# Performance work log

Measured on AMD Instinct MI355X. Metric: run time of the kernel, lower is better.

Reference implementation:

```python
import math
import jax, jax.numpy as jnp
import numpy as np

B, S, H, N = 2, 2048, 2048, 16
HN = H // N
ALPHA = 32.0
MASK_VALUE = 10000.0


def setup_inputs() -> dict:
    key = jax.random.key(0)
    k1, k2, k3, k4, k5 = jax.random.split(key, 5)
    hidden_states = jax.random.normal(k1, (B, S, H), dtype=jnp.float32)
    # causal (left-to-right) multiplicative mask, broadcastable to [b, n, s, s]
    ltor_mask = jnp.tril(jnp.ones((S, S), dtype=jnp.float32))[None, None, :, :]
    # torch Linear params: y = x @ W.T + b
    w_qkv = jax.random.normal(k2, (3 * H, H), dtype=jnp.float32) * (1.0 / math.sqrt(H))
    b_qkv = jnp.zeros((3 * H,), dtype=jnp.float32)
    w_dense = jax.random.normal(k3, (H, H), dtype=jnp.float32) * (1.0 / math.sqrt(H))
    b_dense = jnp.zeros((H,), dtype=jnp.float32)
    return {"hidden_states": hidden_states, "ltor_mask": ltor_mask,
            "w_qkv": w_qkv, "b_qkv": b_qkv, "w_dense": w_dense, "b_dense": b_dense}


def reference(hidden_states, ltor_mask, w_qkv, b_qkv, w_dense, b_dense):
    b, s, h = hidden_states.shape
    # fused qkv projection
    qkv = hidden_states @ w_qkv.T + b_qkv                       # [b, s, 3h]
    q, k, v = jnp.split(qkv, 3, axis=-1)

    def heads(t):  # [b, s, h] -> [b, n, s, hn]
        return t.reshape(b, s, N, HN).transpose(0, 2, 1, 3)

    q, k, v = heads(q), heads(k), heads(v)
    # cogview pb_relax: scale query before matmul
    scores = jnp.einsum('bnsd,bntd->bnst', q / math.sqrt(HN), k)  # [b, n, s, s]
    m = ltor_mask[:, :, -s:]
    scores = scores * m - MASK_VALUE * (1.0 - m)
    # pb_relax max stabilization: per (batch, head) global max of scores/alpha
    scaled = scores / ALPHA
    maxes = jax.lax.stop_gradient(jnp.max(scaled, axis=(-2, -1), keepdims=True))
    scores = (scaled - maxes) * ALPHA
    probs = jax.nn.softmax(scores, axis=-1)
    ctx = jnp.einsum('bnst,bntd->bnsd', probs, v)                # [b, n, s, hn]
    ctx = ctx.transpose(0, 2, 1, 3).reshape(b, s, h)
    out = ctx @ w_dense.T + b_dense
    return out
```

## Files before the change

### kernel.cpp

```cpp
#include <hip/hip_runtime.h>

typedef __bf16 bf16_t;
typedef __bf16 bf16x8 __attribute__((ext_vector_type(8)));
typedef __bf16 bf16x4 __attribute__((ext_vector_type(4)));
typedef float f32x4 __attribute__((ext_vector_type(4)));

#define MFMA16(a, b, c) __builtin_amdgcn_mfma_f32_16x16x32_bf16((a), (b), (c), 0, 0, 0)

__device__ __forceinline__ void gload_lds16(const void* g, void* l) {
  __builtin_amdgcn_global_load_lds(
      (__attribute__((address_space(1))) void*)(g),
      (__attribute__((address_space(3))) void*)(l), 16, 0, 0);
}

__global__ __launch_bounds__(256) void cvt_f32_bf16(const float* __restrict__ in,
                                                    bf16_t* __restrict__ out, int n4) {
  int i = blockIdx.x * 256 + threadIdx.x;
  if (i >= n4) return;
  float4 v = ((const float4*)in)[i];
  bf16x4 o;
  o[0] = (bf16_t)v.x; o[1] = (bf16_t)v.y; o[2] = (bf16_t)v.z; o[3] = (bf16_t)v.w;
  ((bf16x4*)out)[i] = o;
}

template <int EPI>
__global__ __launch_bounds__(256) void gemm_bt(
    const bf16_t* __restrict__ A, const bf16_t* __restrict__ Bw,
    const float* __restrict__ bias,
    void* __restrict__ o0, void* __restrict__ o1, void* __restrict__ o2,
    int M, int N, int K) {
  __shared__ __attribute__((aligned(16))) bf16_t As[128][32];
  __shared__ __attribute__((aligned(16))) bf16_t Bs[128][32];
  const int tid = threadIdx.x;
  const int lane = tid & 63, wave = tid >> 6;
  const int wr = (wave >> 1) * 64, wc = (wave & 1) * 64;
  const int l15 = lane & 15, l4 = lane >> 4;
  const int bm = blockIdx.y * 128, bn = blockIdx.x * 128;

  f32x4 acc[4][4];
#pragma unroll
  for (int i = 0; i < 4; ++i)
#pragma unroll
    for (int j = 0; j < 4; ++j)
#pragma unroll
      for (int r = 0; r < 4; ++r) acc[i][j][r] = 0.0f;

  const int r0 = tid >> 2;
  const int co = (tid & 3) * 8;
  const bf16_t* gA = A + (size_t)(bm + r0) * K + co;
  const bf16_t* gB = Bw + (size_t)(bn + r0) * K + co;

  for (int kk = 0; kk < K; kk += 32) {
    gload_lds16(gA + kk, &As[r0][co]);
    gload_lds16(gA + kk + (size_t)64 * K, &As[r0 + 64][co]);
    gload_lds16(gB + kk, &Bs[r0][co]);
    gload_lds16(gB + kk + (size_t)64 * K, &Bs[r0 + 64][co]);
    asm volatile("s_waitcnt vmcnt(0)" ::: "memory");
    __syncthreads();
    bf16x8 a[4], b[4];
#pragma unroll
    for (int i = 0; i < 4; ++i) a[i] = *(const bf16x8*)(&As[wr + i * 16 + l15][l4 * 8]);
#pragma unroll
    for (int j = 0; j < 4; ++j) b[j] = *(const bf16x8*)(&Bs[wc + j * 16 + l15][l4 * 8]);
#pragma unroll
    for (int i = 0; i < 4; ++i)
#pragma unroll
      for (int j = 0; j < 4; ++j) acc[i][j] = MFMA16(a[i], b[j], acc[i][j]);
    __syncthreads();
  }

  if (EPI == 0) {
    bf16_t* qb = (bf16_t*)o0;
    bf16_t* kb = (bf16_t*)o1;
    bf16_t* vtb = (bf16_t*)o2;
    const int which = bn >> 11;
    const int head = (bn & 2047) >> 7;
#pragma unroll
    for (int i = 0; i < 4; ++i)
#pragma unroll
      for (int j = 0; j < 4; ++j)
#pragma unroll
        for (int r = 0; r < 4; ++r) {
          int m = bm + wr + i * 16 + l4 * 4 + r;
          int n = bn + wc + j * 16 + l15;
          float v = acc[i][j][r] + bias[n];
          int b = m >> 11, s = m & 2047;
          int d = n & 127;
          size_t hb = (size_t)(b * 16 + head);
          if (which == 0) {
            v *= 0.08838834764831845f;
            qb[(hb * 2048 + s) * 128 + d] = (bf16_t)v;
          } else if (which == 1) {
            kb[(hb * 2048 + s) * 128 + d] = (bf16_t)v;
          } else {
            vtb[(hb * 128 + d) * 2048 + s] = (bf16_t)v;
          }
        }
  } else {
    float* O = (float*)o0;
#pragma unroll
    for (int i = 0; i < 4; ++i)
#pragma unroll
      for (int j = 0; j < 4; ++j)
#pragma unroll
        for (int r = 0; r < 4; ++r) {
          int m = bm + wr + i * 16 + l4 * 4 + r;
          int n = bn + wc + j * 16 + l15;
          O[(size_t)m * N + n] = acc[i][j][r] + bias[n];
        }
  }
}

__global__ __launch_bounds__(256) void attn_kernel(
    const bf16_t* __restrict__ qbuf, const bf16_t* __restrict__ kbuf,
    const bf16_t* __restrict__ vtbuf, bf16_t* __restrict__ ctx) {
  __shared__ __attribute__((aligned(16))) bf16_t Ks[64][128];
  __shared__ __attribute__((aligned(16))) bf16_t Vts[128][64];
  __shared__ __attribute__((aligned(16))) bf16_t Ps[4][16][64];

  const int tid = threadIdx.x, lane = tid & 63, w = tid >> 6;
  const int l15 = lane & 15, l4 = lane >> 4;
  const int qt = blockIdx.x, hb = blockIdx.y;
  const int q0 = qt * 64;
  const size_t hoff = (size_t)hb * 2048 * 128;
  const bf16_t* qh = qbuf + hoff;
  const bf16_t* kh = kbuf + hoff;
  const bf16_t* vh = vtbuf + hoff;

  bf16x8 qa[4];
#pragma unroll
  for (int ks = 0; ks < 4; ++ks)
    qa[ks] = *(const bf16x8*)(qh + (size_t)(q0 + w * 16 + l15) * 128 + ks * 32 + l4 * 8);

  f32x4 accO[8];
#pragma unroll
  for (int df = 0; df < 8; ++df)
#pragma unroll
    for (int r = 0; r < 4; ++r) accO[df][r] = 0.0f;
  float mrow[4], lrow[4];
#pragma unroll
  for (int r = 0; r < 4; ++r) { mrow[r] = -1e30f; lrow[r] = 0.0f; }

  const int nt = qt + 1;
  for (int t = 0; t < nt; ++t) {
    const int kv0 = t * 64;
#pragma unroll
    for (int it = 0; it < 4; ++it) {
      int c = tid + it * 256;
      int row = c >> 4, slot = c & 15;
      int sch = slot ^ (row & 7);
      gload_lds16(kh + (size_t)(kv0 + row) * 128 + sch * 8, &Ks[row][slot * 8]);
    }
#pragma unroll
    for (int it = 0; it < 4; ++it) {
      int c = tid + it * 256;
      int row = c >> 3, slot = c & 7;
      int sch = slot ^ (row & 7);
      gload_lds16(vh + (size_t)row * 2048 + kv0 + sch * 8, &Vts[row][slot * 8]);
    }
    asm volatile("s_waitcnt vmcnt(0)" ::: "memory");
    __syncthreads();

    f32x4 sc[4];
#pragma unroll
    for (int nf = 0; nf < 4; ++nf) {
#pragma unroll
      for (int r = 0; r < 4; ++r) sc[nf][r] = 0.0f;
      int row = nf * 16 + l15;
#pragma unroll
      for (int ks = 0; ks < 4; ++ks) {
        int ch = (ks * 4 + l4) ^ (row & 7);
        bf16x8 kf = *(const bf16x8*)(&Ks[row][ch * 8]);
        sc[nf] = MFMA16(qa[ks], kf, sc[nf]);
      }
    }

    if (t == nt - 1) {
#pragma unroll
      for (int nf = 0; nf < 4; ++nf)
#pragma unroll
        for (int r = 0; r < 4; ++r) {
          int qi = q0 + w * 16 + l4 * 4 + r;
          int kv = kv0 + nf * 16 + l15;
          if (kv > qi) sc[nf][r] = -1e30f;
        }
    }

    float tmax[4], rsum[4], scl[4];
#pragma unroll
    for (int r = 0; r < 4; ++r)
      tmax[r] = fmaxf(fmaxf(sc[0][r], sc[1][r]), fmaxf(sc[2][r], sc[3][r]));
#pragma unroll
    for (int msk = 1; msk <= 8; msk <<= 1)
#pragma unroll
      for (int r = 0; r < 4; ++r)
        tmax[r] = fmaxf(tmax[r], __shfl_xor(tmax[r], msk, 64));
#pragma unroll
    for (int r = 0; r < 4; ++r) {
      float mn = fmaxf(mrow[r], tmax[r]);
      scl[r] = __expf(mrow[r] - mn);
      mrow[r] = mn;
      float s0 = 0.0f;
#pragma unroll
      for (int nf = 0; nf < 4; ++nf) {
        float p = __expf(sc[nf][r] - mn);
        sc[nf][r] = p;
        s0 += p;
      }
      rsum[r] = s0;
    }
#pragma unroll
    for (int msk = 1; msk <= 8; msk <<= 1)
#pragma unroll
      for (int r = 0; r < 4; ++r) rsum[r] += __shfl_xor(rsum[r], msk, 64);
#pragma unroll
    for (int r = 0; r < 4; ++r) lrow[r] = lrow[r] * scl[r] + rsum[r];
#pragma unroll
    for (int df = 0; df < 8; ++df)
#pragma unroll
      for (int r = 0; r < 4; ++r) accO[df][r] *= scl[r];

#pragma unroll
    for (int nf = 0; nf < 4; ++nf)
#pragma unroll
      for (int r = 0; r < 4; ++r) {
        int qi = l4 * 4 + r;
        int kv = nf * 16 + l15;
        int ch = (kv >> 3) ^ (qi & 7);
        Ps[w][qi][ch * 8 + (kv & 7)] = (bf16_t)sc[nf][r];
      }

    bf16x8 pa[2];
#pragma unroll
    for (int k2 = 0; k2 < 2; ++k2) {
      int ch = (k2 * 4 + l4) ^ (l15 & 7);
      pa[k2] = *(const bf16x8*)(&Ps[w][l15][ch * 8]);
    }
#pragma unroll
    for (int df = 0; df < 8; ++df) {
      int row = df * 16 + l15;
#pragma unroll
      for (int k2 = 0; k2 < 2; ++k2) {
        int ch = (k2 * 4 + l4) ^ (row & 7);
        bf16x8 vf = *(const bf16x8*)(&Vts[row][ch * 8]);
        accO[df] = MFMA16(pa[k2], vf, accO[df]);
      }
    }
    __syncthreads();
  }

  const int b = hb >> 4, head = hb & 15;
  float inv[4];
#pragma unroll
  for (int r = 0; r < 4; ++r) inv[r] = 1.0f / lrow[r];
#pragma unroll
  for (int df = 0; df < 8; ++df)
#pragma unroll
    for (int r = 0; r < 4; ++r) {
      int s = q0 + w * 16 + l4 * 4 + r;
      int col = head * 128 + df * 16 + l15;
      ctx[((size_t)(b * 2048 + s)) * 2048 + col] = (bf16_t)(accO[df][r] * inv[r]);
    }
}

extern "C" void kernel_launch(void* const* d_in, const int* in_sizes, int n_in,
                              void* d_out, int out_size, void* d_ws, size_t ws_size,
                              hipStream_t stream) {
  const float* hs = (const float*)d_in[0];
  const float* w_qkv = (const float*)d_in[2];
  const float* b_qkv = (const float*)d_in[3];
  const float* w_dense = (const float*)d_in[4];
  const float* b_dense = (const float*)d_in[5];
  float* out = (float*)d_out;

  const size_t SZ_HS = (size_t)4096 * 2048;
  const size_t SZ_WQKV = (size_t)6144 * 2048;
  const size_t SZ_WD = (size_t)2048 * 2048;
  const size_t SZ_H = (size_t)32 * 2048 * 128;

  char* ws = (char*)d_ws;
  bf16_t* A_ = (bf16_t*)ws;
  bf16_t* B_ = (bf16_t*)(ws + 2 * SZ_HS);
  bf16_t* Q_ = (bf16_t*)(ws + 2 * (SZ_HS + SZ_WQKV));
  bf16_t* K_ = Q_ + SZ_H;
  bf16_t* V_ = K_ + SZ_H;

  cvt_f32_bf16<<<(int)(SZ_HS / 4 / 256), 256, 0, stream>>>(hs, A_, (int)(SZ_HS / 4));
  cvt_f32_bf16<<<(int)(SZ_WQKV / 4 / 256), 256, 0, stream>>>(w_qkv, B_, (int)(SZ_WQKV / 4));

  gemm_bt<0><<<dim3(48, 32), 256, 0, stream>>>(A_, B_, b_qkv, Q_, K_, V_, 4096, 6144, 2048);

  cvt_f32_bf16<<<(int)(SZ_WD / 4 / 256), 256, 0, stream>>>(w_dense, A_, (int)(SZ_WD / 4));

  attn_kernel<<<dim3(32, 32), 256, 0, stream>>>(Q_, K_, V_, B_);

  gemm_bt<1><<<dim3(16, 32), 256, 0, stream>>>(B_, A_, b_dense, out, nullptr, nullptr,
                                               4096, 2048, 2048);
}
```

Measured before the change: 518.2 us.

## Restructure attention: 128-row q tiles, paired causal tiles, double-buffered KV, lazy rescale

The attention kernel now uses 512-thread blocks over 128 query rows. Each block handles two query tiles (qt and 15-qt) so every block does the same amount of causal work. K/V tiles are double-buffered in LDS and the next tile is prefetched while the current one computes. Waves whose rows lie entirely above the diagonal skip the tile, and the online-softmax rescale is skipped when the new max stays within a threshold of the running max. This adds LDS use and register pressure and cuts the grid to 256 blocks, which could hurt occupancy.

```diff
diff --git a/kernel.cpp b/kernel.cpp
--- a/kernel.cpp
+++ b/kernel.cpp
@@ -11,6 +11,12 @@
   __builtin_amdgcn_global_load_lds(
       (__attribute__((address_space(1))) void*)(g),
       (__attribute__((address_space(3))) void*)(l), 16, 0, 0);
+}
+
+__device__ __forceinline__ void block_bar() {
+  asm volatile("" ::: "memory");
+  __builtin_amdgcn_s_barrier();
+  asm volatile("" ::: "memory");
 }
 
 __global__ __launch_bounds__(256) void cvt_f32_bf16(const float* __restrict__ in,
@@ -111,156 +117,199 @@
   }
 }
 
-__global__ __launch_bounds__(256) void attn_kernel(
+__global__ __launch_bounds__(512) void attn_kernel(
     const bf16_t* __restrict__ qbuf, const bf16_t* __restrict__ kbuf,
     const bf16_t* __restrict__ vtbuf, bf16_t* __restrict__ ctx) {
-  __shared__ __attribute__((aligned(16))) bf16_t Ks[64][128];
-  __shared__ __attribute__((aligned(16))) bf16_t Vts[128][64];
-  __shared__ __attribute__((aligned(16))) bf16_t Ps[4][16][64];
+  __shared__ __attribute__((aligned(16))) bf16_t Ks[2][64][128];
+  __shared__ __attribute__((aligned(16))) bf16_t Vts[2][128][64];
+  __shared__ __attribute__((aligned(16))) bf16_t Ps[8][16][64];
 
   const int tid = threadIdx.x, lane = tid & 63, w = tid >> 6;
   const int l15 = lane & 15, l4 = lane >> 4;
-  const int qt = blockIdx.x, hb = blockIdx.y;
-  const int q0 = qt * 64;
+  const int hb = blockIdx.y;
   const size_t hoff = (size_t)hb * 2048 * 128;
   const bf16_t* qh = qbuf + hoff;
   const bf16_t* kh = kbuf + hoff;
   const bf16_t* vh = vtbuf + hoff;
-
-  bf16x8 qa[4];
-#pragma unroll
-  for (int ks = 0; ks < 4; ++ks)
-    qa[ks] = *(const bf16x8*)(qh + (size_t)(q0 + w * 16 + l15) * 128 + ks * 32 + l4 * 8);
-
-  f32x4 accO[8];
-#pragma unroll
-  for (int df = 0; df < 8; ++df)
-#pragma unroll
-    for (int r = 0; r < 4; ++r) accO[df][r] = 0.0f;
-  float mrow[4], lrow[4];
-#pragma unroll
-  for (int r = 0; r < 4; ++r) { mrow[r] = -1e30f; lrow[r] = 0.0f; }
-
-  const int nt = qt + 1;
-  for (int t = 0; t < nt; ++t) {
-    const int kv0 = t * 64;
-#pragma unroll
-    for (int it = 0; it < 4; ++it) {
-      int c = tid + it * 256;
-      int row = c >> 4, slot = c & 15;
-      int sch = slot ^ (row & 7);
-      gload_lds16(kh + (size_t)(kv0 + row) * 128 + sch * 8, &Ks[row][slot * 8]);
+  const int b = hb >> 4, head = hb & 15;
+
+  const int kr0 = tid >> 4, ks0 = tid & 15;
+  const int vr0 = tid >> 3, vs0 = tid & 7;
+
+  int buf = 0;
+
+#pragma unroll 1
+  for (int phase = 0; phase < 2; ++phase) {
+    const int qt = phase == 0 ? blockIdx.x : 15 - blockIdx.x;
+    const int q0 = qt * 128;
+    const int nt = 2 * qt + 2;
+
+    bf16x8 qa[4];
+#pragma unroll
+    for (int ks = 0; ks < 4; ++ks)
+      qa[ks] = *(const bf16x8*)(qh + (size_t)(q0 + w * 16 + l15) * 128 + ks * 32 + l4 * 8);
+
+    f32x4 accO[8];
+#pragma unroll
+    for (int df = 0; df < 8; ++df)
+#pragma unroll
+      for (int r = 0; r < 4; ++r) accO[df][r] = 0.0f;
+    float mrow[4], lrow[4];
+#pragma unroll
+    for (int r = 0; r < 4; ++r) { mrow[r] = -1e30f; lrow[r] = 0.0f; }
+
+    {
+      const int kv0 = 0;
+#pragma unroll
+      for (int it = 0; it < 2; ++it) {
+        int row = kr0 + it * 32, sch = ks0 ^ (row & 7);
+        gload_lds16(kh + (size_t)(kv0 + row) * 128 + sch * 8, &Ks[buf][row][ks0 * 8]);
+      }
+#pragma unroll
+      for (int it = 0; it < 2; ++it) {
+        int row = vr0 + it * 64, sch = vs0 ^ (row & 7);
+        gload_lds16(vh + (size_t)row * 2048 + kv0 + sch * 8, &Vts[buf][row][vs0 * 8]);
+      }
     }
-#pragma unroll
-    for (int it = 0; it < 4; ++it) {
-      int c = tid + it * 256;
-      int row = c >> 3, slot = c & 7;
-      int sch = slot ^ (row & 7);
-      gload_lds16(vh + (size_t)row * 2048 + kv0 + sch * 8, &Vts[row][slot * 8]);
+
+#pragma unroll 1
+    for (int t = 0; t < nt; ++t) {
+      const int kv0 = t * 64;
+      if (t + 1 < nt) {
+        const int kvn = (t + 1) * 64;
+        const int nb = buf ^ 1;
+#pragma unroll
+        for (int it = 0; it < 2; ++it) {
+          int row = kr0 + it * 32, sch = ks0 ^ (row & 7);
+          gload_lds16(kh + (size_t)(kvn + row) * 128 + sch * 8, &Ks[nb][row][ks0 * 8]);
+        }
+#pragma unroll
+        for (int it = 0; it < 2; ++it) {
+          int row = vr0 + it * 64, sch = vs0 ^ (row & 7);
+          gload_lds16(vh + (size_t)row * 2048 + kvn + sch * 8, &Vts[nb][row][vs0 * 8]);
+        }
+        asm volatile("s_waitcnt vmcnt(4)" ::: "memory");
+      } else {
+        asm volatile("s_waitcnt vmcnt(0)" ::: "memory");
+      }
+      block_bar();
+
+      const bool active = (kv0 <= q0 + w * 16 + 15);
+      if (active) {
+        f32x4 sc[4];
+#pragma unroll
+        for (int nf = 0; nf < 4; ++nf) {
+#pragma unroll
+          for (int r = 0; r < 4; ++r) sc[nf][r] = 0.0f;
+          int row = nf * 16 + l15;
+#pragma unroll
+          for (int ks = 0; ks < 4; ++ks) {
+            int ch = (ks * 4 + l4) ^ (row & 7);
+            bf16x8 kf = *(const bf16x8*)(&Ks[buf][row][ch * 8]);
+            sc[nf] = MFMA16(qa[ks], kf, sc[nf]);
+          }
+        }
+
+        if (kv0 + 63 > q0 + w * 16) {
+#pragma unroll
+          for (int nf = 0; nf < 4; ++nf)
+#pragma unroll
+            for (int r = 0; r < 4; ++r) {
+              int qi = q0 + w * 16 + l4 * 4 + r;
+              int kv = kv0 + nf * 16 + l15;
+              if (kv > qi) sc[nf][r] = -1e30f;
+            }
+        }
+
+        float tmax[4];
+#pragma unroll
+        for (int r = 0; r < 4; ++r)
+          tmax[r] = fmaxf(fmaxf(sc[0][r], sc[1][r]), fmaxf(sc[2][r], sc[3][r]));
+#pragma unroll
+        for (int msk = 1; msk <= 8; msk <<= 1)
+#pragma unroll
+          for (int r = 0; r < 4; ++r)
+            tmax[r] = fmaxf(tmax[r], __shfl_xor(tmax[r], msk, 64));
+
+        bool defer = __all(tmax[0] <= mrow[0] + 8.0f && tmax[1] <= mrow[1] + 8.0f &&
+                           tmax[2] <= mrow[2] + 8.0f && tmax[3] <= mrow[3] + 8.0f);
+        if (!defer) {
+          float scl[4];
+#pragma unroll
+          for (int r = 0; r < 4; ++r) {
+            float mn = fmaxf(mrow[r], tmax[r]);
+            scl[r] = __expf(mrow[r] - mn);
+            mrow[r] = mn;
+            lrow[r] *= scl[r];
+          }
+#pragma unroll
+          for (int df = 0; df < 8; ++df)
+#pragma unroll
+            for (int r = 0; r < 4; ++r) accO[df][r] *= scl[r];
+        }
+
+        float rsum[4];
+#pragma unroll
+        for (int r = 0; r < 4; ++r) {
+          float s0 = 0.0f;
+#pragma unroll
+          for (int nf = 0; nf < 4; ++nf) {
+            float p = __expf(sc[nf][r] - mrow[r]);
+            sc[nf][r] = p;
+            s0 += p;
+          }
+          rsum[r] = s0;
+        }
+#pragma unroll
+        for (int msk = 1; msk <= 8; msk <<= 1)
+#pragma unroll
+          for (int r = 0; r < 4; ++r) rsum[r] += __shfl_xor(rsum[r], msk, 64);
+#pragma unroll
+        for (int r = 0; r < 4; ++r) lrow[r] += rsum[r];
+
+#pragma unroll
+        for (int nf = 0; nf < 4; ++nf)
+#pragma unroll
+          for (int r = 0; r < 4; ++r) {
+            int qi = l4 * 4 + r;
+            int kv = nf * 16 + l15;
+            int ch = (kv >> 3) ^ (qi & 7);
+            Ps[w][qi][ch * 8 + (kv & 7)] = (bf16_t)sc[nf][r];
+          }
+
+        bf16x8 pa[2];
+#pragma unroll
+        for (int k2 = 0; k2 < 2; ++k2) {
+          int ch = (k2 * 4 + l4) ^ (l15 & 7);
+          pa[k2] = *(const bf16x8*)(&Ps[w][l15][ch * 8]);
+        }
+#pragma unroll
+        for (int df = 0; df < 8; ++df) {
+          int row = df * 16 + l15;
+#pragma unroll
+          for (int k2 = 0; k2 < 2; ++k2) {
+            int ch = (k2 * 4 + l4) ^ (row & 7);
+            bf16x8 vf = *(const bf16x8*)(&Vts[buf][row][ch * 8]);
+            accO[df] = MFMA16(pa[k2], vf, accO[df]);
+          }
+        }
+      }
+      block_bar();
+      buf ^= 1;
     }
-    asm volatile("s_waitcnt vmcnt(0)" ::: "memory");
-    __syncthreads();
-
-    f32x4 sc[4];
-#pragma unroll
-    for (int nf = 0; nf < 4; ++nf) {
-#pragma unroll
-      for (int r = 0; r < 4; ++r) sc[nf][r] = 0.0f;
-      int row = nf * 16 + l15;
-#pragma unroll
-      for (int ks = 0; ks < 4; ++ks) {
-        int ch = (ks * 4 + l4) ^ (row & 7);
-        bf16x8 kf = *(const bf16x8*)(&Ks[row][ch * 8]);
-        sc[nf] = MFMA16(qa[ks], kf, sc[nf]);
-      }
-    }
-
-    if (t == nt - 1) {
-#pragma unroll
-      for (int nf = 0; nf < 4; ++nf)
-#pragma unroll
-        for (int r = 0; r < 4; ++r) {
-          int qi = q0 + w * 16 + l4 * 4 + r;
-          int kv = kv0 + nf * 16 + l15;
-          if (kv > qi) sc[nf][r] = -1e30f;
-        }
-    }
-
-    float tmax[4], rsum[4], scl[4];
-#pragma unroll
-    for (int r = 0; r < 4; ++r)
-      tmax[r] = fmaxf(fmaxf(sc[0][r], sc[1][r]), fmaxf(sc[2][r], sc[3][r]));
-#pragma unroll
-    for (int msk = 1; msk <= 8; msk <<= 1)
-#pragma unroll
-      for (int r = 0; r < 4; ++r)
-        tmax[r] = fmaxf(tmax[r], __shfl_xor(tmax[r], msk, 64));
-#pragma unroll
-    for (int r = 0; r < 4; ++r) {
-      float mn = fmaxf(mrow[r], tmax[r]);
-      scl[r] = __expf(mrow[r] - mn);
-      mrow[r] = mn;
-      float s0 = 0.0f;
-#pragma unroll
-      for (int nf = 0; nf < 4; ++nf) {
-        float p = __expf(sc[nf][r] - mn);
-        sc[nf][r] = p;
-        s0 += p;
-      }
-      rsum[r] = s0;
-    }
-#pragma unroll
-    for (int msk = 1; msk <= 8; msk <<= 1)
-#pragma unroll
-      for (int r = 0; r < 4; ++r) rsum[r] += __shfl_xor(rsum[r], msk, 64);
-#pragma unroll
-    for (int r = 0; r < 4; ++r) lrow[r] = lrow[r] * scl[r] + rsum[r];
+
+    float inv[4];
+#pragma unroll
+    for (int r = 0; r < 4; ++r) inv[r] = 1.0f / lrow[r];
 #pragma unroll
     for (int df = 0; df < 8; ++df)
 #pragma unroll
-      for (int r = 0; r < 4; ++r) accO[df][r] *= scl[r];
-
-#pragma unroll
-    for (int nf = 0; nf < 4; ++nf)
-#pragma unroll
       for (int r = 0; r < 4; ++r) {
-        int qi = l4 * 4 + r;
-        int kv = nf * 16 + l15;
-        int ch = (kv >> 3) ^ (qi & 7);
-        Ps[w][qi][ch * 8 + (kv & 7)] = (bf16_t)sc[nf][r];
-      }
-
-    bf16x8 pa[2];
-#pragma unroll
-    for (int k2 = 0; k2 < 2; ++k2) {
-      int ch = (k2 * 4 + l4) ^ (l15 & 7);
-      pa[k2] = *(const bf16x8*)(&Ps[w][l15][ch * 8]);
-    }
-#pragma unroll
-    for (int df = 0; df < 8; ++df) {
-      int row = df * 16 + l15;
-#pragma unroll
-      for (int k2 = 0; k2 < 2; ++k2) {
-        int ch = (k2 * 4 + l4) ^ (row & 7);
-        bf16x8 vf = *(const bf16x8*)(&Vts[row][ch * 8]);
-        accO[df] = MFMA16(pa[k2], vf, accO[df]);
-      }
-    }
-    __syncthreads();
+        int s = q0 + w * 16 + l4 * 4 + r;
+        int col = head * 128 + df * 16 + l15;
+        ctx[((size_t)(b * 2048 + s)) * 2048 + col] = (bf16_t)(accO[df][r] * inv[r]);
+      }
   }
-
-  const int b = hb >> 4, head = hb & 15;
-  float inv[4];
-#pragma unroll
-  for (int r = 0; r < 4; ++r) inv[r] = 1.0f / lrow[r];
-#pragma unroll
-  for (int df = 0; df < 8; ++df)
-#pragma unroll
-    for (int r = 0; r < 4; ++r) {
-      int s = q0 + w * 16 + l4 * 4 + r;
-      int col = head * 128 + df * 16 + l15;
-      ctx[((size_t)(b * 2048 + s)) * 2048 + col] = (bf16_t)(accO[df][r] * inv[r]);
-    }
 }
 
 extern "C" void kernel_launch(void* const* d_in, const int* in_sizes, int n_in,
@@ -292,7 +341,7 @@
 
   cvt_f32_bf16<<<(int)(SZ_WD / 4 / 256), 256, 0, stream>>>(w_dense, A_, (int)(SZ_WD / 4));
 
-  attn_kernel<<<dim3(32, 32), 256, 0, stream>>>(Q_, K_, V_, B_);
+  attn_kernel<<<dim3(8, 32), 512, 0, stream>>>(Q_, K_, V_, B_);
 
   gemm_bt<1><<<dim3(16, 32), 256, 0, stream>>>(B_, A_, b_dense, out, nullptr, nullptr,
                                                4096, 2048, 2048);
```

After: 461.8 us. 1.12x faster.
